# Optimization experiments

Hardware: AMD Instinct MI355X
Metric: run time of the kernel (lower is better)

Reference implementation:

```python
import jax, jax.numpy as jnp
import numpy as np
from functools import partial

B, S, D_IN, H = 8, 2048, 1024, 1024
V = 50257
NUM_CODEWORDS, EMB_DIM = 256, 16
NUM_NEURONS, TOP_K = 64, 16  # top_k = sparsity(0.25) * 64
TILE_ROWS = 16
NUM_TILES = H // TILE_ROWS  # 64 -> decoder out_features = 1024
FREQS = (1.0, 2.0, 4.0)
MAX_LEN = 1024


def setup_inputs() -> dict:
    key = jax.random.key(0)
    ks = jax.random.split(key, 16)
    s = 0.02
    return {
        "inputs": jax.random.normal(ks[0], (B, S, D_IN), jnp.float32),
        "Wt": jax.random.normal(ks[1], (H, D_IN), jnp.float32) * s,
        "bt": jnp.zeros((H,), jnp.float32),
        "Wq": jax.random.normal(ks[2], (H, H), jnp.float32) * s,
        "bq": jnp.zeros((H,), jnp.float32),
        "Wk": jax.random.normal(ks[3], (H, H), jnp.float32) * s,
        "bk": jnp.zeros((H,), jnp.float32),
        "Wv": jax.random.normal(ks[4], (H, H), jnp.float32) * s,
        "bv": jnp.zeros((H,), jnp.float32),
        "Wo": jax.random.normal(ks[5], (D_IN, H), jnp.float32) * s,
        "bo": jnp.zeros((D_IN,), jnp.float32),
        "codebook": jax.random.normal(ks[6], (NUM_CODEWORDS, EMB_DIM), jnp.float32) * s,
        "instructions": jax.random.randint(ks[7], (NUM_TILES * TILE_ROWS, D_IN // EMB_DIM), 0, NUM_CODEWORDS),
        "W_lm": jax.random.normal(ks[8], (V, NUM_TILES * TILE_ROWS), jnp.float32) * s,
        "b_lm": jnp.zeros((V,), jnp.float32),
    }


def _positional_bias(seq_len):
    # AttentionBasisSynthesizer: sin/cos atoms at freqs (1,2,4), gains=1, shifts=0
    ang = 2.0 * jnp.pi * jnp.arange(seq_len, dtype=jnp.float32) / MAX_LEN
    bias = jnp.zeros((seq_len,), jnp.float32)
    for f in FREQS:
        bias = bias + jnp.sin(f * ang) + jnp.cos(f * ang)
    return bias  # [S]


def _forward(inputs, Wt, bt, Wq, bq, Wk, bk, Wv, bv, Wo, bo, codebook, instructions, W_lm, b_lm):
    tokens = inputs @ Wt.T + bt                       # [B,S,H]
    q = tokens @ Wq.T + bq
    k = tokens @ Wk.T + bk
    v = tokens @ Wv.T + bv
    # per-step KV-cache loop == causal attention over prefix; vectorize
    scores = jnp.einsum("bqh,bkh->bqk", q, k) / jnp.sqrt(jnp.float32(H))
    scores = scores + _positional_bias(S)[None, None, :]
    i = jnp.arange(S)
    causal = i[:, None] >= i[None, :]                 # [S,S]
    scores = jnp.where(causal[None], scores, -jnp.inf)
    attn = jnp.einsum("bqk,bkh->bqh", jax.nn.softmax(scores, axis=-1), v)  # [B,S,H]
    # sparse routing: group into NUM_NEURONS neurons, keep top-k by L2 norm,
    # softmax weights over kept neurons, straight-through combine with dense path
    g = attn.reshape(B, S, NUM_NEURONS, H // NUM_NEURONS)
    sc = jnp.sqrt(jnp.sum(g * g, axis=-1))            # [B,S,N]
    vals, idx = jax.lax.top_k(sc, TOP_K)              # [B,S,K]
    w = jax.nn.softmax(vals, axis=-1)
    onehot = jax.nn.one_hot(idx, NUM_NEURONS, dtype=attn.dtype)  # [B,S,K,N]
    wfull = jnp.einsum("bsk,bskn->bsn", w, onehot)    # [B,S,N]
    combined = (g * wfull[..., None]).reshape(B, S, H)
    combined = combined + (attn - jax.lax.stop_gradient(attn))  # straight-through
    dec_in = combined @ Wo.T + bo                     # [B,S,D_IN]
    x = jnp.mean(dec_in, axis=1)                      # [B,D_IN]
    # DemopackDecoder: weight rows assembled from codebook via instruction indices
    W_dec = codebook[instructions].reshape(NUM_TILES * TILE_ROWS, D_IN)
    hidden = x @ W_dec.T                              # [B, 1024]
    return hidden @ W_lm.T + b_lm                     # [B, V]


def reference(inputs, Wt, bt, Wq, bq, Wk, bk, Wv, bv, Wo, bo, codebook, instructions, W_lm, b_lm):
    return _forward(inputs, Wt, bt, Wq, bq, Wk, bk, Wv, bv, Wo, bo, codebook, instructions, W_lm, b_lm)
```

## Files before the change

### kernel.cpp

```cpp
#include <hip/hip_runtime.h>
#include <cstdint>
#include <cstddef>

#define B_   8
#define S_   2048
#define DIN_ 1024
#define H_   1024
#define V_   50257

typedef unsigned short ushort_t;
typedef __bf16 bf16x8 __attribute__((ext_vector_type(8)));
typedef float  f32x4  __attribute__((ext_vector_type(4)));

__device__ __forceinline__ ushort_t f2bf(float x) {
    unsigned u = __float_as_uint(x);
    u = (u + 0x7fffu + ((u >> 16) & 1u)) >> 16;
    return (ushort_t)u;
}

__device__ __forceinline__ void async16(const void* g, void* s) {
    __builtin_amdgcn_global_load_lds(
        (const __attribute__((address_space(1))) unsigned int*)g,
        (__attribute__((address_space(3))) unsigned int*)s, 16, 0, 0);
}

__device__ __forceinline__ float wredmax(float v) {
#pragma unroll
    for (int o = 32; o; o >>= 1) v = fmaxf(v, __shfl_xor(v, o));
    return v;
}
__device__ __forceinline__ float wredsum(float v) {
#pragma unroll
    for (int o = 32; o; o >>= 1) v += __shfl_xor(v, o);
    return v;
}

__global__ void f2bf_vec(const float* __restrict__ in, ushort_t* __restrict__ out, int n4) {
    int i = blockIdx.x * 256 + threadIdx.x;
    if (i >= n4) return;
    float4 f = ((const float4*)in)[i];
    ushort4 u;
    u.x = f2bf(f.x); u.y = f2bf(f.y); u.z = f2bf(f.z); u.w = f2bf(f.w);
    ((ushort4*)out)[i] = u;
}

__global__ void f2bf_w3(const float* __restrict__ Wq, const float* __restrict__ Wk,
                        const float* __restrict__ Wv, ushort_t* __restrict__ out) {
    int i = blockIdx.x * 256 + threadIdx.x;
    int w = i >> 18, off = i & 262143;
    const float* src = w == 0 ? Wq : (w == 1 ? Wk : Wv);
    float4 f = ((const float4*)src)[off];
    ushort4 u;
    u.x = f2bf(f.x); u.y = f2bf(f.y); u.z = f2bf(f.z); u.w = f2bf(f.w);
    ((ushort4*)(out + (size_t)w * 1048576))[off] = u;
}

__global__ void pos_bias_kernel(float* __restrict__ bias) {
    int k = blockIdx.x * 256 + threadIdx.x;
    if (k >= S_) return;
    float ang = 6.283185307179586f * (float)k / 1024.0f;
    float b = 0.f;
    b += sinf(1.f * ang) + cosf(1.f * ang);
    b += sinf(2.f * ang) + cosf(2.f * ang);
    b += sinf(4.f * ang) + cosf(4.f * ang);
    bias[k] = b;
}

__global__ __launch_bounds__(256)
void transpose_wt(const float* __restrict__ Wt, ushort_t* __restrict__ wtT) {
    __shared__ float t[64][65];
    int k0 = blockIdx.x * 64, i0 = blockIdx.y * 64;
    int tx = threadIdx.x & 63, ty = threadIdx.x >> 6;
#pragma unroll
    for (int j = 0; j < 16; j++) {
        int k = ty * 16 + j;
        t[k][tx] = Wt[(size_t)(k0 + k) * DIN_ + i0 + tx];
    }
    __syncthreads();
#pragma unroll
    for (int j = 0; j < 16; j++) {
        int i = ty * 16 + j;
        wtT[(size_t)(i0 + i) * H_ + k0 + tx] = f2bf(t[tx][i]);
    }
}

__global__ __launch_bounds__(256)
void bcomb_kernel(const float* __restrict__ Wq, const float* __restrict__ Wk,
                  const float* __restrict__ Wv, const float* __restrict__ bq,
                  const float* __restrict__ bk, const float* __restrict__ bv,
                  const float* __restrict__ bt, float* __restrict__ bcomb) {
    int wave = threadIdx.x >> 6, lane = threadIdx.x & 63;
    int j = blockIdx.x * 4 + wave;
    const float* W  = j < 1024 ? Wq : (j < 2048 ? Wk : Wv);
    const float* bb = j < 1024 ? bq : (j < 2048 ? bk : bv);
    int rowj = j & 1023;
    const float4* wr4 = (const float4*)(W + (size_t)rowj * 1024);
    const float4* bt4 = (const float4*)bt;
    float s = 0.f;
#pragma unroll
    for (int c = 0; c < 4; c++) {
        float4 w = wr4[c * 64 + lane];
        float4 b = bt4[c * 64 + lane];
        s += w.x * b.x + w.y * b.y + w.z * b.z + w.w * b.w;
    }
    s = wredsum(s);
    if (lane == 0) bcomb[j] = s + bb[rowj];
}

template <int OUT_BF16>
__global__ __launch_bounds__(256)
void gemm_bt(const ushort_t* __restrict__ A, int lda,
             const ushort_t* __restrict__ Bt, int ldb,
             void* __restrict__ Cv, int ldc, int K, const float* __restrict__ bias) {
    int bn = blockIdx.x, bm = blockIdx.y;
    __shared__ ushort_t As[128 * 32];
    __shared__ ushort_t Bs[128 * 32];
    int tid = threadIdx.x, wave = tid >> 6, lane = tid & 63;
    int wr = wave >> 1, wc = wave & 1;
    int nkt = K >> 5;
    int srow = lane >> 2, scol = (lane & 3) * 8;
    size_t arow0 = (size_t)bm * 128, brow0 = (size_t)bn * 128;
    f32x4 acc[4][4];
#pragma unroll
    for (int m = 0; m < 4; m++)
#pragma unroll
        for (int n = 0; n < 4; n++) acc[m][n] = f32x4{0.f, 0.f, 0.f, 0.f};
    for (int kt = 0; kt < nkt; ++kt) {
        int k0 = kt * 32;
#pragma unroll
        for (int i = 0; i < 2; i++) {
            int reg = wave * 2 + i;
            int row = reg * 16 + srow;
            async16(A + (arow0 + row) * (size_t)lda + k0 + scol, (ushort_t*)As + reg * 512);
            async16(Bt + (brow0 + row) * (size_t)ldb + k0 + scol, (ushort_t*)Bs + reg * 512);
        }
        __syncthreads();
        bf16x8 af[4], bfr[4];
#pragma unroll
        for (int m = 0; m < 4; m++)
            af[m] = *(const bf16x8*)&As[(wr * 64 + m * 16 + (lane & 15)) * 32 + (lane >> 4) * 8];
#pragma unroll
        for (int n = 0; n < 4; n++)
            bfr[n] = *(const bf16x8*)&Bs[(wc * 64 + n * 16 + (lane & 15)) * 32 + (lane >> 4) * 8];
#pragma unroll
        for (int m = 0; m < 4; m++)
#pragma unroll
            for (int n = 0; n < 4; n++)
                acc[m][n] = __builtin_amdgcn_mfma_f32_16x16x32_bf16(af[m], bfr[n], acc[m][n], 0, 0, 0);
        __syncthreads();
    }
    int rl = (lane >> 4) * 4, cl = lane & 15;
#pragma unroll
    for (int m = 0; m < 4; m++)
#pragma unroll
        for (int n = 0; n < 4; n++) {
            int col = bn * 128 + wc * 64 + n * 16 + cl;
            float badd = bias ? bias[col] : 0.f;
#pragma unroll
            for (int r = 0; r < 4; r++) {
                int row = bm * 128 + wr * 64 + m * 16 + rl + r;
                float v = acc[m][n][r] + badd;
                size_t off = (size_t)row * ldc + col;
                if (OUT_BF16) ((ushort_t*)Cv)[off] = f2bf(v);
                else          ((float*)Cv)[off] = v;
            }
        }
}

template <int OUT_BF16, int CAUSAL_SKIP, int KLIM>
__global__ __launch_bounds__(512, 2)
void gemm256(const ushort_t* __restrict__ A, size_t sAb, int lda,
             const ushort_t* __restrict__ Bt, size_t sBb, int ldb,
             void* __restrict__ Cv, size_t sCb, int ldc,
             int K, const float* __restrict__ bias, int nbn, int nwg) {
    extern __shared__ char lds[];
    int orig = blockIdx.x, bz = blockIdx.y;
    int qq = nwg >> 3, rr8 = nwg & 7;
    int xcd = orig & 7, bidx = orig >> 3;
    int wgid = (xcd < rr8 ? xcd * (qq + 1) : rr8 * (qq + 1) + (xcd - rr8) * qq) + bidx;
    int bm = wgid / nbn, bn = wgid - bm * nbn;
    if (CAUSAL_SKIP && bn > bm) return;

    const ushort_t* Ab = A + (size_t)bz * sAb;
    const ushort_t* Bb = Bt + (size_t)bz * sBb;
    int tid = threadIdx.x, wave = tid >> 6, lane = tid & 63;
    int wr = wave >> 2, wc = wave & 3;

    int kmax = K;
    if (KLIM) { int km = (bm + 1) * 256; kmax = km < K ? km : K; }
    int nkt = kmax >> 6;

    int srow = wave * 8 + (lane >> 3);
    int sswz = ((lane & 7) ^ (lane >> 3)) * 8;
    const ushort_t* Ag = Ab + ((size_t)bm * 256 + srow) * (size_t)lda + sswz;
    const ushort_t* Bg = Bb + ((size_t)bn * 256 + srow) * (size_t)ldb + sswz;
    int sdst = wave * 1024;

    int fr = lane & 15, g = lane >> 4;
    int kx = (fr >> 2) & 1;
    int gsw = (g ^ (fr & 3)) * 16;
    int aoff = wr * 16384 + fr * 128 + gsw;
    int boff = 32768 + (wc >> 1) * 16384 + ((wc & 1) * 64 + fr) * 128 + gsw;
    int ks0 = kx << 6, ks1 = (kx ^ 1) << 6;

    f32x4 acc[8][4];
#pragma unroll
    for (int m = 0; m < 8; m++)
#pragma unroll
        for (int n = 0; n < 4; n++) acc[m][n] = f32x4{0.f, 0.f, 0.f, 0.f};

#define STG_A(t, h, bo)                                                        \
    do {                                                                       \
        async16(Ag + (size_t)((h) * 128) * lda + (t) * 64,                     \
                lds + (bo) + (h) * 16384 + sdst);                              \
        async16(Ag + (size_t)((h) * 128 + 64) * lda + (t) * 64,                \
                lds + (bo) + (h) * 16384 + 8192 + sdst);                       \
    } while (0)
#define STG_B(t, h, bo)                                                        \
    do {                                                                       \
        async16(Bg + (size_t)((h) * 128) * ldb + (t) * 64,                     \
                lds + (bo) + 32768 + (h) * 16384 + sdst);                      \
        async16(Bg + (size_t)((h) * 128 + 64) * ldb + (t) * 64,                \
                lds + (bo) + 32768 + (h) * 16384 + 8192 + sdst);               \
    } while (0)

    STG_A(0, 0, 0); STG_A(0, 1, 0); STG_B(0, 0, 0); STG_B(0, 1, 0);
    STG_A(1, 0, 65536); STG_A(1, 1, 65536); STG_B(1, 0, 65536); STG_B(1, 1, 65536);
    asm volatile("s_waitcnt vmcnt(8)" ::: "memory");
    __builtin_amdgcn_sched_barrier(0);
    __builtin_amdgcn_s_barrier();
    __builtin_amdgcn_sched_barrier(0);

    bf16x8 af03[4][2], af47[4][2], bf01[2][2], bf23[2][2];
#pragma unroll
    for (int mf = 0; mf < 4; mf++) {
        af03[mf][0] = *(const bf16x8*)(lds + aoff + mf * 2048 + ks0);
        af03[mf][1] = *(const bf16x8*)(lds + aoff + mf * 2048 + ks1);
    }
#pragma unroll
    for (int nf = 0; nf < 2; nf++) {
        bf01[nf][0] = *(const bf16x8*)(lds + boff + nf * 2048 + ks0);
        bf01[nf][1] = *(const bf16x8*)(lds + boff + nf * 2048 + ks1);
    }

    int bufo = 0;
    for (int t = 0; t < nkt; ++t, bufo ^= 65536) {
        int nb = bufo ^ 65536;
#pragma unroll
        for (int mf = 0; mf < 4; mf++) {
            af47[mf][0] = *(const bf16x8*)(lds + bufo + aoff + (mf + 4) * 2048 + ks0);
            af47[mf][1] = *(const bf16x8*)(lds + bufo + aoff + (mf + 4) * 2048 + ks1);
        }
#pragma unroll
        for (int nf = 0; nf < 2; nf++) {
            bf23[nf][0] = *(const bf16x8*)(lds + bufo + boff + (nf + 2) * 2048 + ks0);
            bf23[nf][1] = *(const bf16x8*)(lds + bufo + boff + (nf + 2) * 2048 + ks1);
        }
        __builtin_amdgcn_s_setprio(1);
#pragma unroll
        for (int mf = 0; mf < 4; mf++)
#pragma unroll
            for (int nf = 0; nf < 2; nf++) {
                acc[mf][nf] = __builtin_amdgcn_mfma_f32_16x16x32_bf16(af03[mf][0], bf01[nf][0], acc[mf][nf], 0, 0, 0);
                acc[mf][nf] = __builtin_amdgcn_mfma_f32_16x16x32_bf16(af03[mf][1], bf01[nf][1], acc[mf][nf], 0, 0, 0);
            }
        __builtin_amdgcn_s_setprio(0);
        __builtin_amdgcn_sched_barrier(0);
        __builtin_amdgcn_s_barrier();
        __builtin_amdgcn_sched_barrier(0);

        __builtin_amdgcn_s_setprio(1);
#pragma unroll
        for (int mf = 0; mf < 4; mf++)
#pragma unroll
            for (int nf = 0; nf < 2; nf++) {
                acc[mf + 4][nf] = __builtin_amdgcn_mfma_f32_16x16x32_bf16(af47[mf][0], bf01[nf][0], acc[mf + 4][nf], 0, 0, 0);
                acc[mf + 4][nf] = __builtin_amdgcn_mfma_f32_16x16x32_bf16(af47[mf][1], bf01[nf][1], acc[mf + 4][nf], 0, 0, 0);
            }
        __builtin_amdgcn_s_setprio(0);
        __builtin_amdgcn_sched_barrier(0);
        __builtin_amdgcn_s_barrier();
        __builtin_amdgcn_sched_barrier(0);

        if (t + 2 < nkt) STG_A(t + 2, 0, bufo);
        __builtin_amdgcn_s_setprio(1);
#pragma unroll
        for (int mf = 0; mf < 4; mf++)
#pragma unroll
            for (int nf = 0; nf < 2; nf++) {
                acc[mf][nf + 2] = __builtin_amdgcn_mfma_f32_16x16x32_bf16(af03[mf][0], bf23[nf][0], acc[mf][nf + 2], 0, 0, 0);
                acc[mf][nf + 2] = __builtin_amdgcn_mfma_f32_16x16x32_bf16(af03[mf][1], bf23[nf][1], acc[mf][nf + 2], 0, 0, 0);
            }
        __builtin_amdgcn_s_setprio(0);
        __builtin_amdgcn_sched_barrier(0);
        if (t + 1 < nkt) {
            if (t + 2 < nkt) { asm volatile("s_waitcnt vmcnt(2)" ::: "memory"); }
            else             { asm volatile("s_waitcnt vmcnt(0)" ::: "memory"); }
        }
        __builtin_amdgcn_s_barrier();
        __builtin_amdgcn_sched_barrier(0);

        if (t + 1 < nkt) {
#pragma unroll
            for (int mf = 0; mf < 4; mf++) {
                af03[mf][0] = *(const bf16x8*)(lds + nb + aoff + mf * 2048 + ks0);
                af03[mf][1] = *(const bf16x8*)(lds + nb + aoff + mf * 2048 + ks1);
            }
#pragma unroll
            for (int nf = 0; nf < 2; nf++) {
                bf01[nf][0] = *(const bf16x8*)(lds + nb + boff + nf * 2048 + ks0);
                bf01[nf][1] = *(const bf16x8*)(lds + nb + boff + nf * 2048 + ks1);
            }
        }
        if (t + 2 < nkt) { STG_A(t + 2, 1, bufo); STG_B(t + 2, 0, bufo); STG_B(t + 2, 1, bufo); }
        __builtin_amdgcn_s_setprio(1);
#pragma unroll
        for (int mf = 0; mf < 4; mf++)
#pragma unroll
            for (int nf = 0; nf < 2; nf++) {
                acc[mf + 4][nf + 2] = __builtin_amdgcn_mfma_f32_16x16x32_bf16(af47[mf][0], bf23[nf][0], acc[mf + 4][nf + 2], 0, 0, 0);
                acc[mf + 4][nf + 2] = __builtin_amdgcn_mfma_f32_16x16x32_bf16(af47[mf][1], bf23[nf][1], acc[mf + 4][nf + 2], 0, 0, 0);
            }
        __builtin_amdgcn_s_setprio(0);
        __builtin_amdgcn_sched_barrier(0);
        __builtin_amdgcn_s_barrier();
        __builtin_amdgcn_sched_barrier(0);
    }
#undef STG_A
#undef STG_B

    int rl = (lane >> 4) * 4, cl = lane & 15;
#pragma unroll
    for (int mf = 0; mf < 8; mf++)
#pragma unroll
        for (int nf = 0; nf < 4; nf++) {
            int col = bn * 256 + wc * 64 + nf * 16 + cl;
            float badd = bias ? bias[col] : 0.f;
#pragma unroll
            for (int r = 0; r < 4; r++) {
                int row = bm * 256 + wr * 128 + mf * 16 + rl + r;
                float v = acc[mf][nf][r] + badd;
                size_t off = (size_t)bz * sCb + (size_t)row * ldc + col;
                if (OUT_BF16) ((ushort_t*)Cv)[off] = f2bf(v);
                else          ((float*)Cv)[off] = v;
            }
        }
}

__global__ __launch_bounds__(256)
void transpose_v(const ushort_t* __restrict__ qkv, ushort_t* __restrict__ vT) {
    __shared__ ushort_t t[64][66];
    int b = blockIdx.z;
    int s0 = blockIdx.x * 64, h0 = blockIdx.y * 64;
    int tx = threadIdx.x & 63, ty = threadIdx.x >> 6;
#pragma unroll
    for (int i = 0; i < 16; i++) {
        int s = ty * 16 + i;
        t[s][tx] = qkv[((size_t)b * S_ + s0 + s) * 3072 + 2048 + h0 + tx];
    }
    __syncthreads();
#pragma unroll
    for (int i = 0; i < 16; i++) {
        int h = ty * 16 + i;
        vT[((size_t)b * H_ + h0 + h) * S_ + s0 + tx] = t[tx][h];
    }
}

__global__ __launch_bounds__(256)
void softmax_kernel(const float* __restrict__ scores, ushort_t* __restrict__ P,
                    const float* __restrict__ bias) {
    __shared__ float srs[S_];
    __shared__ float red[8];
    int q = blockIdx.x, b = blockIdx.y;
    int L = q + 1;
    int tid = threadIdx.x;
    const float* srow = scores + ((size_t)b * S_ + q) * S_;
    const float scale = 0.03125f;

    float lm = -3e38f;
    for (int k = tid; k < L; k += 256) {
        float s = srow[k] * scale + bias[k];
        srs[k] = s;
        lm = fmaxf(lm, s);
    }
    lm = wredmax(lm);
    if ((tid & 63) == 0) red[tid >> 6] = lm;
    __syncthreads();
    float m = fmaxf(fmaxf(red[0], red[1]), fmaxf(red[2], red[3]));

    float ls = 0.f;
    for (int k = tid; k < L; k += 256) {
        float e = __expf(srs[k] - m);
        srs[k] = e;
        ls += e;
    }
    ls = wredsum(ls);
    if ((tid & 63) == 0) red[4 + (tid >> 6)] = ls;
    __syncthreads();
    float invs = 1.f / (red[4] + red[5] + red[6] + red[7]);

    int kz = ((q >> 8) + 1) * 256;
    ushort_t* prow = P + ((size_t)b * S_ + q) * S_;
    for (int k = tid; k < kz; k += 256)
        prow[k] = (k < L) ? f2bf(srs[k] * invs) : (ushort_t)0;
}

__global__ __launch_bounds__(256)
void routing_kernel(const float* __restrict__ attn, ushort_t* __restrict__ combined) {
    int wave = threadIdx.x >> 6, lane = threadIdx.x & 63;
    size_t row = (size_t)blockIdx.x * 4 + wave;
    const float4* a4 = (const float4*)(attn + row * H_);
    float4 x0 = a4[lane * 4 + 0], x1 = a4[lane * 4 + 1];
    float4 x2 = a4[lane * 4 + 2], x3 = a4[lane * 4 + 3];
    float ss = x0.x * x0.x + x0.y * x0.y + x0.z * x0.z + x0.w * x0.w
             + x1.x * x1.x + x1.y * x1.y + x1.z * x1.z + x1.w * x1.w
             + x2.x * x2.x + x2.y * x2.y + x2.z * x2.z + x2.w * x2.w
             + x3.x * x3.x + x3.y * x3.y + x3.z * x3.z + x3.w * x3.w;
    float sc = sqrtf(ss);

    float v = sc, thr = 0.f, mx = 0.f;
#pragma unroll
    for (int i = 0; i < 16; i++) {
        float mm = wredmax(v);
        if (i == 0) mx = mm;
        thr = mm;
        if (v == mm) v = -1e30f;
    }
    float e = (sc >= thr) ? __expf(sc - mx) : 0.f;
    float se = wredsum(e);
    float w = e / se;

    const float xs[16] = {x0.x, x0.y, x0.z, x0.w, x1.x, x1.y, x1.z, x1.w,
                          x2.x, x2.y, x2.z, x2.w, x3.x, x3.y, x3.z, x3.w};
    union { ushort_t u[16]; uint4 q[2]; } pk;
#pragma unroll
    for (int j = 0; j < 16; j++) pk.u[j] = f2bf(xs[j] * w);
    uint4* dst = (uint4*)(combined + row * H_ + lane * 16);
    dst[0] = pk.q[0];
    dst[1] = pk.q[1];
}

__global__ void cmean_part(const ushort_t* __restrict__ comb, float* __restrict__ part) {
    int d = blockIdx.x * 256 + threadIdx.x;
    int sc = blockIdx.y, b = blockIdx.z;
    const ushort_t* p = comb + ((size_t)b * S_ + sc * 128) * H_ + d;
    float s = 0.f;
    for (int i = 0; i < 128; i++) s += __uint_as_float((unsigned)p[(size_t)i * H_] << 16);
    part[((size_t)b * 16 + sc) * H_ + d] = s;
}

__global__ void cmean_final(const float* __restrict__ part, float* __restrict__ cm) {
    int idx = blockIdx.x * 256 + threadIdx.x;
    int b = idx >> 10, d = idx & 1023;
    float s = 0.f;
#pragma unroll
    for (int c = 0; c < 16; c++) s += part[((size_t)b * 16 + c) * DIN_ + d];
    cm[idx] = s * (1.0f / 2048.0f);
}

__global__ __launch_bounds__(256)
void xgemv(const float* __restrict__ cm, const float* __restrict__ Wo,
           const float* __restrict__ bo, float* __restrict__ x) {
    int wave = threadIdx.x >> 6, lane = threadIdx.x & 63;
    int i = blockIdx.x * 4 + wave;
    const float4* wr4 = (const float4*)(Wo + (size_t)i * H_);
    float4 w[4];
#pragma unroll
    for (int c = 0; c < 4; c++) w[c] = wr4[c * 64 + lane];
    float accv[B_];
#pragma unroll
    for (int b = 0; b < B_; b++) {
        const float4* c4 = (const float4*)(cm + (size_t)b * H_);
        float s = 0.f;
#pragma unroll
        for (int c = 0; c < 4; c++) {
            float4 h = c4[c * 64 + lane];
            s += w[c].x * h.x + w[c].y * h.y + w[c].z * h.z + w[c].w * h.w;
        }
        accv[b] = wredsum(s);
    }
    if (lane == 0) {
        float bi = bo[i];
#pragma unroll
        for (int b = 0; b < B_; b++) x[(size_t)b * DIN_ + i] = accv[b] + bi;
    }
}

__global__ __launch_bounds__(64)
void decode_hidden(const float* __restrict__ x, const float* __restrict__ codebook,
                   const int* __restrict__ instr, float* __restrict__ hidden) {
    int r = blockIdx.x;
    int lane = threadIdx.x;
    int idx = instr[r * 64 + lane];
    const float4* cw = (const float4*)(codebook + (size_t)idx * 16);
    float4 c0 = cw[0], c1 = cw[1], c2 = cw[2], c3 = cw[3];
    float acc[B_];
#pragma unroll
    for (int b = 0; b < B_; b++) {
        const float4* xb = (const float4*)(x + (size_t)b * DIN_ + lane * 16);
        float4 h0 = xb[0], h1 = xb[1], h2 = xb[2], h3 = xb[3];
        acc[b] = c0.x * h0.x + c0.y * h0.y + c0.z * h0.z + c0.w * h0.w
               + c1.x * h1.x + c1.y * h1.y + c1.z * h1.z + c1.w * h1.w
               + c2.x * h2.x + c2.y * h2.y + c2.z * h2.z + c2.w * h2.w
               + c3.x * h3.x + c3.y * h3.y + c3.z * h3.z + c3.w * h3.w;
    }
#pragma unroll
    for (int b = 0; b < B_; b++) acc[b] = wredsum(acc[b]);
    if (lane == 0) {
#pragma unroll
        for (int b = 0; b < B_; b++) hidden[(size_t)b * 1024 + r] = acc[b];
    }
}

__global__ __launch_bounds__(256)
void lm_head(const float* __restrict__ Wlm, const float* __restrict__ hidden,
             const float* __restrict__ blm, float* __restrict__ out) {
    int wave = threadIdx.x >> 6, lane = threadIdx.x & 63;
    for (int v = blockIdx.x * 4 + wave; v < V_; v += gridDim.x * 4) {
        const float4* wrow = (const float4*)(Wlm + (size_t)v * 1024);
        float acc[B_];
#pragma unroll
        for (int b = 0; b < B_; b++) acc[b] = 0.f;
#pragma unroll
        for (int rr = 0; rr < 4; rr++) {
            float4 wv = wrow[rr * 64 + lane];
#pragma unroll
            for (int b = 0; b < B_; b++) {
                float4 hv = ((const float4*)hidden)[b * 256 + rr * 64 + lane];
                acc[b] += wv.x * hv.x + wv.y * hv.y + wv.z * hv.z + wv.w * hv.w;
            }
        }
#pragma unroll
        for (int b = 0; b < B_; b++) acc[b] = wredsum(acc[b]);
        if (lane == 0) {
            float bl = blm[v];
#pragma unroll
            for (int b = 0; b < B_; b++) out[(size_t)b * V_ + v] = acc[b] + bl;
        }
    }
}

extern "C" void kernel_launch(void* const* d_in, const int* in_sizes, int n_in,
                              void* d_out, int out_size, void* d_ws, size_t ws_size,
                              hipStream_t stream) {
    const float* inputs = (const float*)d_in[0];
    const float* Wt  = (const float*)d_in[1];
    const float* bt  = (const float*)d_in[2];
    const float* Wq  = (const float*)d_in[3];
    const float* bq  = (const float*)d_in[4];
    const float* Wk  = (const float*)d_in[5];
    const float* bk  = (const float*)d_in[6];
    const float* Wv  = (const float*)d_in[7];
    const float* bv  = (const float*)d_in[8];
    const float* Wo  = (const float*)d_in[9];
    const float* bo  = (const float*)d_in[10];
    const float* codebook = (const float*)d_in[11];
    const int*   instructions = (const int*)d_in[12];
    const float* Wlm = (const float*)d_in[13];
    const float* blm = (const float*)d_in[14];
    float* out = (float*)d_out;

    (void)hipFuncSetAttribute(reinterpret_cast<const void*>(&gemm256<1, 0, 0>),
                              hipFuncAttributeMaxDynamicSharedMemorySize, 131072);
    (void)hipFuncSetAttribute(reinterpret_cast<const void*>(&gemm256<0, 1, 0>),
                              hipFuncAttributeMaxDynamicSharedMemorySize, 131072);
    (void)hipFuncSetAttribute(reinterpret_cast<const void*>(&gemm256<0, 0, 1>),
                              hipFuncAttributeMaxDynamicSharedMemorySize, 131072);

    const size_t MB = 1024 * 1024;
    char* ws = (char*)d_ws;
    ushort_t* wqkv_bf = (ushort_t*)(ws + 0);
    ushort_t* wtT_bf  = (ushort_t*)(ws + 6 * MB);
    ushort_t* wcomb   = (ushort_t*)(ws + 8 * MB);
    float* bcomb  = (float*)(ws + 14 * MB);
    float* pbias  = (float*)(ws + 14 * MB + 64 * 1024);
    float* cm     = (float*)(ws + 14 * MB + 128 * 1024);
    float* xbuf   = (float*)(ws + 14 * MB + 192 * 1024);
    float* hidden = (float*)(ws + 14 * MB + 256 * 1024);
    float* part   = (float*)(ws + 14 * MB + 512 * 1024);
    ushort_t* inbf   = (ushort_t*)(ws + 16 * MB);
    ushort_t* qkv    = (ushort_t*)(ws + 48 * MB);
    ushort_t* vT     = (ushort_t*)(ws + 144 * MB);
    float* scores    = (float*)(ws + 176 * MB);
    ushort_t* P      = (ushort_t*)(ws + 304 * MB);
    float* attn      = (float*)(ws + 48 * MB);
    ushort_t* combined = (ushort_t*)(ws + 176 * MB);

    f2bf_vec<<<16384, 256, 0, stream>>>(inputs, inbf, 4194304);
    f2bf_w3<<<3072, 256, 0, stream>>>(Wq, Wk, Wv, wqkv_bf);
    transpose_wt<<<dim3(16, 16), 256, 0, stream>>>(Wt, wtT_bf);
    bcomb_kernel<<<768, 256, 0, stream>>>(Wq, Wk, Wv, bq, bk, bv, bt, bcomb);
    pos_bias_kernel<<<8, 256, 0, stream>>>(pbias);

    gemm_bt<1><<<dim3(8, 24), 256, 0, stream>>>(wqkv_bf, 1024, wtT_bf, 1024,
                                                wcomb, 1024, 1024, nullptr);

    gemm256<1, 0, 0><<<dim3(768, 1), 512, 131072, stream>>>(
        inbf, 0, 1024, wcomb, 0, 1024, qkv, 0, 3072, 1024, bcomb, 12, 768);

    transpose_v<<<dim3(32, 16, 8), 256, 0, stream>>>(qkv, vT);

    gemm256<0, 1, 0><<<dim3(64, 8), 512, 131072, stream>>>(
        qkv, (size_t)S_ * 3072, 3072, qkv + 1024, (size_t)S_ * 3072, 3072,
        scores, (size_t)S_ * S_, S_, 1024, nullptr, 8, 64);

    softmax_kernel<<<dim3(S_, B_), 256, 0, stream>>>(scores, P, pbias);

    gemm256<0, 0, 1><<<dim3(32, 8), 512, 131072, stream>>>(
        P, (size_t)S_ * S_, S_, vT, (size_t)H_ * S_, S_,
        attn, (size_t)S_ * H_, H_, S_, nullptr, 4, 32);

    routing_kernel<<<4096, 256, 0, stream>>>(attn, combined);

    cmean_part<<<dim3(4, 16, 8), 256, 0, stream>>>(combined, part);
    cmean_final<<<32, 256, 0, stream>>>(part, cm);
    xgemv<<<256, 256, 0, stream>>>(cm, Wo, bo, xbuf);

    decode_hidden<<<1024, 64, 0, stream>>>(xbuf, codebook, instructions, hidden);

    lm_head<<<2048, 256, 0, stream>>>(Wlm, hidden, blm, out);
}
```

Before: 459.8 us.

## Compact causal QK grid and split-K the PV GEMM for load balance

The scores GEMM now launches only the 36 lower-triangular tiles per batch, computing each tile's coordinates from a triangular index, so no workgroups are launched just to exit. The P·V GEMM splits rows past 1024 into two K halves written to separate buffers, ordered so heavy and light tiles balance across 48 workgroups per batch. The routing kernel adds the second partial back in. An extra LDS waitcnt is added before one barrier, which may cost a little; the partial buffer adds memory traffic.

```diff
diff --git a/kernel.cpp b/kernel.cpp
--- a/kernel.cpp
+++ b/kernel.cpp
@@ -167,33 +167,57 @@
         }
 }
 
-template <int OUT_BF16, int CAUSAL_SKIP, int KLIM>
+template <int OUT_BF16, int MODE>
 __global__ __launch_bounds__(512, 2)
 void gemm256(const ushort_t* __restrict__ A, size_t sAb, int lda,
              const ushort_t* __restrict__ Bt, size_t sBb, int ldb,
              void* __restrict__ Cv, size_t sCb, int ldc,
-             int K, const float* __restrict__ bias, int nbn, int nwg) {
+             int K, const float* __restrict__ bias, int nbn, int nwg,
+             float* __restrict__ Cv2) {
     extern __shared__ char lds[];
-    int orig = blockIdx.x, bz = blockIdx.y;
-    int qq = nwg >> 3, rr8 = nwg & 7;
-    int xcd = orig & 7, bidx = orig >> 3;
-    int wgid = (xcd < rr8 ? xcd * (qq + 1) : rr8 * (qq + 1) + (xcd - rr8) * qq) + bidx;
-    int bm = wgid / nbn, bn = wgid - bm * nbn;
-    if (CAUSAL_SKIP && bn > bm) return;
+    int bz = blockIdx.y;
+    int bm, bn, koff = 0, nkt;
+    void* Cuse = Cv;
+    size_t sCuse = sCb;
+    if (MODE == 2) {
+        int x = blockIdx.x;
+        if (x < 32) {
+            bm = x >> 2; bn = x & 3;
+            int km = (bm + 1) * 256; if (km > 1024) km = 1024;
+            nkt = km >> 6;
+        } else {
+            int j = x - 32;
+            bm = 7 - (j >> 2); bn = j & 3;
+            koff = 1024;
+            nkt = ((bm + 1) * 256 - 1024) >> 6;
+            Cuse = Cv2;
+            sCuse = (size_t)1024 * 1024;
+        }
+    } else {
+        int orig = blockIdx.x;
+        int qq = nwg >> 3, rr8 = nwg & 7;
+        int xcd = orig & 7, bidx = orig >> 3;
+        int wgid = (xcd < rr8 ? xcd * (qq + 1) : rr8 * (qq + 1) + (xcd - rr8) * qq) + bidx;
+        if (MODE == 1) {
+            int w = wgid;
+            bm = 0;
+            while ((bm + 1) * (bm + 2) / 2 <= w) bm++;
+            bn = w - bm * (bm + 1) / 2;
+        } else {
+            bm = wgid / nbn; bn = wgid - bm * nbn;
+        }
+        nkt = K >> 6;
+    }
 
     const ushort_t* Ab = A + (size_t)bz * sAb;
     const ushort_t* Bb = Bt + (size_t)bz * sBb;
     int tid = threadIdx.x, wave = tid >> 6, lane = tid & 63;
     int wr = wave >> 2, wc = wave & 3;
 
-    int kmax = K;
-    if (KLIM) { int km = (bm + 1) * 256; kmax = km < K ? km : K; }
-    int nkt = kmax >> 6;
-
     int srow = wave * 8 + (lane >> 3);
     int sswz = ((lane & 7) ^ (lane >> 3)) * 8;
-    const ushort_t* Ag = Ab + ((size_t)bm * 256 + srow) * (size_t)lda + sswz;
-    const ushort_t* Bg = Bb + ((size_t)bn * 256 + srow) * (size_t)ldb + sswz;
+    const ushort_t* Ag = Ab + ((size_t)bm * 256 + srow) * (size_t)lda + sswz + koff;
+    const ushort_t* Bg = Bb + ((size_t)bn * 256 + srow) * (size_t)ldb + sswz + koff;
     int sdst = wave * 1024;
 
     int fr = lane & 15, g = lane >> 4;
@@ -266,6 +290,8 @@
             }
         __builtin_amdgcn_s_setprio(0);
         __builtin_amdgcn_sched_barrier(0);
+        asm volatile("s_waitcnt lgkmcnt(0)" ::: "memory");
+        __builtin_amdgcn_sched_barrier(0);
         __builtin_amdgcn_s_barrier();
         __builtin_amdgcn_sched_barrier(0);
 
@@ -340,9 +366,9 @@
             for (int r = 0; r < 4; r++) {
                 int row = bm * 256 + wr * 128 + mf * 16 + rl + r;
                 float v = acc[mf][nf][r] + badd;
-                size_t off = (size_t)bz * sCb + (size_t)row * ldc + col;
-                if (OUT_BF16) ((ushort_t*)Cv)[off] = f2bf(v);
-                else          ((float*)Cv)[off] = v;
+                size_t off = (size_t)bz * sCuse + (size_t)row * ldc + col;
+                if (OUT_BF16) ((ushort_t*)Cuse)[off] = f2bf(v);
+                else          ((float*)Cuse)[off] = v;
             }
         }
 }
@@ -406,12 +432,24 @@
 }
 
 __global__ __launch_bounds__(256)
-void routing_kernel(const float* __restrict__ attn, ushort_t* __restrict__ combined) {
+void routing_kernel(const float* __restrict__ attn, const float* __restrict__ attn2,
+                    ushort_t* __restrict__ combined) {
     int wave = threadIdx.x >> 6, lane = threadIdx.x & 63;
     size_t row = (size_t)blockIdx.x * 4 + wave;
     const float4* a4 = (const float4*)(attn + row * H_);
     float4 x0 = a4[lane * 4 + 0], x1 = a4[lane * 4 + 1];
     float4 x2 = a4[lane * 4 + 2], x3 = a4[lane * 4 + 3];
+    int q = (int)(row & 2047);
+    if (q >= 1024) {
+        size_t b = row >> 11;
+        const float4* a2 = (const float4*)(attn2 + ((b * 1024 + (size_t)(q - 1024)) * H_));
+        float4 y0 = a2[lane * 4 + 0], y1 = a2[lane * 4 + 1];
+        float4 y2 = a2[lane * 4 + 2], y3 = a2[lane * 4 + 3];
+        x0.x += y0.x; x0.y += y0.y; x0.z += y0.z; x0.w += y0.w;
+        x1.x += y1.x; x1.y += y1.y; x1.z += y1.z; x1.w += y1.w;
+        x2.x += y2.x; x2.y += y2.y; x2.z += y2.z; x2.w += y2.w;
+        x3.x += y3.x; x3.y += y3.y; x3.z += y3.z; x3.w += y3.w;
+    }
     float ss = x0.x * x0.x + x0.y * x0.y + x0.z * x0.z + x0.w * x0.w
              + x1.x * x1.x + x1.y * x1.y + x1.z * x1.z + x1.w * x1.w
              + x2.x * x2.x + x2.y * x2.y + x2.z * x2.z + x2.w * x2.w
@@ -432,12 +470,12 @@
 
     const float xs[16] = {x0.x, x0.y, x0.z, x0.w, x1.x, x1.y, x1.z, x1.w,
                           x2.x, x2.y, x2.z, x2.w, x3.x, x3.y, x3.z, x3.w};
-    union { ushort_t u[16]; uint4 q[2]; } pk;
+    union { ushort_t u[16]; uint4 q4[2]; } pk;
 #pragma unroll
     for (int j = 0; j < 16; j++) pk.u[j] = f2bf(xs[j] * w);
     uint4* dst = (uint4*)(combined + row * H_ + lane * 16);
-    dst[0] = pk.q[0];
-    dst[1] = pk.q[1];
+    dst[0] = pk.q4[0];
+    dst[1] = pk.q4[1];
 }
 
 __global__ void cmean_part(const ushort_t* __restrict__ comb, float* __restrict__ part) {
@@ -560,11 +598,11 @@
     const float* blm = (const float*)d_in[14];
     float* out = (float*)d_out;
 
-    (void)hipFuncSetAttribute(reinterpret_cast<const void*>(&gemm256<1, 0, 0>),
+    (void)hipFuncSetAttribute(reinterpret_cast<const void*>(&gemm256<1, 0>),
                               hipFuncAttributeMaxDynamicSharedMemorySize, 131072);
-    (void)hipFuncSetAttribute(reinterpret_cast<const void*>(&gemm256<0, 1, 0>),
+    (void)hipFuncSetAttribute(reinterpret_cast<const void*>(&gemm256<0, 1>),
                               hipFuncAttributeMaxDynamicSharedMemorySize, 131072);
-    (void)hipFuncSetAttribute(reinterpret_cast<const void*>(&gemm256<0, 0, 1>),
+    (void)hipFuncSetAttribute(reinterpret_cast<const void*>(&gemm256<0, 2>),
                               hipFuncAttributeMaxDynamicSharedMemorySize, 131072);
 
     const size_t MB = 1024 * 1024;
@@ -584,6 +622,7 @@
     float* scores    = (float*)(ws + 176 * MB);
     ushort_t* P      = (ushort_t*)(ws + 304 * MB);
     float* attn      = (float*)(ws + 48 * MB);
+    float* attn2     = (float*)(ws + 112 * MB);
     ushort_t* combined = (ushort_t*)(ws + 176 * MB);
 
     f2bf_vec<<<16384, 256, 0, stream>>>(inputs, inbf, 4194304);
@@ -595,22 +634,22 @@
     gemm_bt<1><<<dim3(8, 24), 256, 0, stream>>>(wqkv_bf, 1024, wtT_bf, 1024,
                                                 wcomb, 1024, 1024, nullptr);
 
-    gemm256<1, 0, 0><<<dim3(768, 1), 512, 131072, stream>>>(
-        inbf, 0, 1024, wcomb, 0, 1024, qkv, 0, 3072, 1024, bcomb, 12, 768);
+    gemm256<1, 0><<<dim3(768, 1), 512, 131072, stream>>>(
+        inbf, 0, 1024, wcomb, 0, 1024, qkv, 0, 3072, 1024, bcomb, 12, 768, nullptr);
 
     transpose_v<<<dim3(32, 16, 8), 256, 0, stream>>>(qkv, vT);
 
-    gemm256<0, 1, 0><<<dim3(64, 8), 512, 131072, stream>>>(
+    gemm256<0, 1><<<dim3(36, 8), 512, 131072, stream>>>(
         qkv, (size_t)S_ * 3072, 3072, qkv + 1024, (size_t)S_ * 3072, 3072,
-        scores, (size_t)S_ * S_, S_, 1024, nullptr, 8, 64);
+        scores, (size_t)S_ * S_, S_, 1024, nullptr, 36, 36, nullptr);
 
     softmax_kernel<<<dim3(S_, B_), 256, 0, stream>>>(scores, P, pbias);
 
-    gemm256<0, 0, 1><<<dim3(32, 8), 512, 131072, stream>>>(
+    gemm256<0, 2><<<dim3(48, 8), 512, 131072, stream>>>(
         P, (size_t)S_ * S_, S_, vT, (size_t)H_ * S_, S_,
-        attn, (size_t)S_ * H_, H_, S_, nullptr, 4, 32);
-
-    routing_kernel<<<4096, 256, 0, stream>>>(attn, combined);
+        attn, (size_t)S_ * H_, H_, S_, nullptr, 0, 0, attn2 - (size_t)1024 * 1024);
+
+    routing_kernel<<<4096, 256, 0, stream>>>(attn, attn2, combined);
 
     cmean_part<<<dim3(4, 16, 8), 256, 0, stream>>>(combined, part);
     cmean_final<<<32, 256, 0, stream>>>(part, cm);
```

New measurement: 458.2 us. No clear change (-0.3%).
